# Performance work log

Hardware: AMD Instinct MI355X
Metric: run time of the kernel (lower is better)

Reference implementation:

```python
import jax, jax.numpy as jnp
import numpy as np

N = 50000        # nodes
E = 1600000      # edges (avg degree 32)
F_IN = 512       # input features
HID = 8          # hidden per head (hardcoded in module)
HEADS = 8        # in_head (hardcoded in module)
CLS = 16         # num_classes
NEG_SLOPE = 0.2  # PyG GATConv default


def setup_inputs() -> dict:
    key = jax.random.key(0)
    ks = jax.random.split(key, 12)
    s = 0.05
    return {
        "x": jax.random.normal(ks[0], (N, F_IN), dtype=jnp.float32),
        "edge_index": jax.random.randint(ks[1], (2, E), 0, N, dtype=jnp.int64),
        "W1": jax.random.normal(ks[2], (F_IN, HEADS * HID), dtype=jnp.float32) * s,
        "att_src1": jax.random.normal(ks[3], (HEADS, HID), dtype=jnp.float32) * s,
        "att_dst1": jax.random.normal(ks[4], (HEADS, HID), dtype=jnp.float32) * s,
        "bias1": jax.random.normal(ks[5], (HEADS * HID,), dtype=jnp.float32) * s,
        "W2": jax.random.normal(ks[6], (HEADS * HID, CLS), dtype=jnp.float32) * s,
        "att_src2": jax.random.normal(ks[7], (1, CLS), dtype=jnp.float32) * s,
        "att_dst2": jax.random.normal(ks[8], (1, CLS), dtype=jnp.float32) * s,
        "bias2": jax.random.normal(ks[9], (CLS,), dtype=jnp.float32) * s,
    }


def _gat_conv(x, src, dst, W, att_src, att_dst, bias, n, heads, ch, concat):
    # Linear projection: [n, heads, ch]
    h = (x @ W).reshape(n, heads, ch)
    # Per-node attention logits (PyG style): alpha_src/dst = sum(h * a)
    a_src = jnp.einsum("nhc,hc->nh", h, att_src)  # [n, heads]
    a_dst = jnp.einsum("nhc,hc->nh", h, att_dst)
    # Per-edge raw score, leaky_relu, then segment softmax over incoming edges per dst
    e = jax.nn.leaky_relu(a_src[src] + a_dst[dst], NEG_SLOPE)  # [Etot, heads]
    m = jax.ops.segment_max(e, dst, num_segments=n)            # [n, heads]
    w = jnp.exp(e - m[dst])
    den = jax.ops.segment_sum(w, dst, num_segments=n)
    alpha = w / den[dst]                                        # [Etot, heads]
    # Scatter-aggregate weighted source features
    out = jax.ops.segment_sum(h[src] * alpha[..., None], dst, num_segments=n)  # [n, heads, ch]
    out = out.reshape(n, heads * ch) if concat else out.mean(axis=1)
    return out + bias


def reference(x, edge_index, W1, att_src1, att_dst1, bias1, W2, att_src2, att_dst2, bias2):
    n = x.shape[0]
    # PyG GATConv adds self-loops by default
    loops = jnp.arange(n, dtype=edge_index.dtype)
    src = jnp.concatenate([edge_index[0], loops])
    dst = jnp.concatenate([edge_index[1], loops])
    # dropout(p=0.6) is identity in eval mode
    h = _gat_conv(x, src, dst, W1, att_src1, att_dst1, bias1, n, HEADS, HID, True)
    h = jax.nn.elu(h)
    out = _gat_conv(h, src, dst, W2, att_src2, att_dst2, bias2, n, 1, CLS, False)
    return jax.nn.log_softmax(out, axis=1)
```

## Files before the change

kernel.cpp:

```cpp
#include <hip/hip_runtime.h>
#include <cstddef>

#define N_NODES 50000
#define N_EDGES 1600000
#define N_ETOT  (N_EDGES + N_NODES)
#define F_IN    512
#define HEADS   8
#define HID     8
#define CLS     16

#define NBUCK   196
#define BCAP    12288
#define CHUNKA  4096
#define NB_GEMM1 782
#define NB_BUCKA 391

typedef float v4 __attribute__((ext_vector_type(4)));
typedef float v2 __attribute__((ext_vector_type(2)));
typedef unsigned short us4 __attribute__((ext_vector_type(4)));
typedef unsigned int u4 __attribute__((ext_vector_type(4)));
typedef short bfrag __attribute__((ext_vector_type(8)));
typedef float ffrag __attribute__((ext_vector_type(4)));

__device__ inline float b2f_lo(unsigned int u) { return __uint_as_float(u << 16); }
__device__ inline float b2f_hi(unsigned int u) { return __uint_as_float(u & 0xffff0000u); }
__device__ inline unsigned short f2b(float f) {
  unsigned int x = __float_as_uint(f);
  unsigned int r = (x + 0x7fffu + ((x >> 16) & 1u)) >> 16;
  return (unsigned short)r;
}

__global__ __launch_bounds__(256) void w1t_kernel(
    const float* __restrict__ W, unsigned short* __restrict__ WT,
    int* __restrict__ gcur) {
  int t = threadIdx.x;
  if (blockIdx.x == 128) {
    if (t < NBUCK) gcur[t] = 0;
    return;
  }
  int i = blockIdx.x * 256 + t;
  int k = i >> 6, n = i & 63;
  WT[n * F_IN + k] = f2b(W[i]);
}

__global__ __launch_bounds__(256) void gemm1_bucketA_kernel(
    const float* __restrict__ x, const unsigned short* __restrict__ W1bT,
    const float* __restrict__ att_src, const float* __restrict__ att_dst,
    unsigned short* __restrict__ h1b, float* __restrict__ a_src,
    float* __restrict__ a_dst, int nrows,
    const int* __restrict__ src_idx, const int* __restrict__ dst_idx,
    int* __restrict__ gcur, int* __restrict__ abuck) {
  __shared__ unsigned short xsb[64][72];
  __shared__ unsigned short wsb[64][72];
  __shared__ int hist[NBUCK];
  __shared__ int base[NBUCK];
  __shared__ int cur[NBUCK];
  int t = threadIdx.x;

  if (blockIdx.x >= NB_GEMM1) {
    if (t < NBUCK) hist[t] = 0;
    __syncthreads();
    int blk = blockIdx.x - NB_GEMM1;
    int e0 = blk * CHUNKA;
    int eend = e0 + CHUNKA;
    if (eend > N_EDGES) eend = N_EDGES;
    for (int e = e0 + t; e < eend; e += 256)
      atomicAdd(&hist[(unsigned)dst_idx[e] >> 8], 1);
    __syncthreads();
    if (t < NBUCK) {
      int c = hist[t];
      base[t] = c ? atomicAdd(&gcur[t], c) : 0;
      cur[t] = 0;
    }
    __syncthreads();
    for (int e = e0 + t; e < eend; e += 256) {
      int s = src_idx[e];
      int d = dst_idx[e];
      int b = (unsigned)d >> 8;
      int r = atomicAdd(&cur[b], 1);
      abuck[b * BCAP + base[b] + r] = (s << 8) | (d & 255);
    }
    return;
  }

  int lane = t & 63;
  int w = t >> 6;
  int row0 = blockIdx.x * 64;
  ffrag acc[4];
  acc[0] = 0.f; acc[1] = 0.f; acc[2] = 0.f; acc[3] = 0.f;

  int mrow = lane & 15;
  int koff = (lane >> 4) * 8;

  for (int kt = 0; kt < 8; ++kt) {
    int k0 = kt * 64;
#pragma unroll
    for (int r = 0; r < 4; ++r) {
      int slot = t + r * 256;
      int m = slot >> 4;
      int k4 = (slot & 15) * 4;
      v4 v = 0.f;
      int grow = row0 + m;
      if (grow < nrows) v = *(const v4*)(x + (size_t)grow * F_IN + k0 + k4);
      us4 o;
      o.x = f2b(v[0]); o.y = f2b(v[1]); o.z = f2b(v[2]); o.w = f2b(v[3]);
      *(us4*)&xsb[m][k4] = o;
    }
#pragma unroll
    for (int r = 0; r < 2; ++r) {
      int slot = t + r * 256;
      int nn = slot >> 3;
      int k8 = (slot & 7) * 8;
      *(bfrag*)&wsb[nn][k8] = *(const bfrag*)(W1bT + nn * F_IN + k0 + k8);
    }
    __syncthreads();
#pragma unroll
    for (int kk = 0; kk < 64; kk += 32) {
      bfrag a = *(const bfrag*)&xsb[w * 16 + mrow][kk + koff];
#pragma unroll
      for (int tt = 0; tt < 4; ++tt) {
        bfrag b = *(const bfrag*)&wsb[tt * 16 + mrow][kk + koff];
        acc[tt] = __builtin_amdgcn_mfma_f32_16x16x32_bf16(a, b, acc[tt], 0, 0, 0);
      }
    }
    __syncthreads();
  }
  int c = lane & 15, q = lane >> 4;
  float as_[4], ad_[4];
#pragma unroll
  for (int tt = 0; tt < 4; ++tt) {
    as_[tt] = att_src[tt * 16 + c];
    ad_[tt] = att_dst[tt * 16 + c];
  }
#pragma unroll
  for (int r = 0; r < 4; ++r) {
    int grow = row0 + w * 16 + q * 4 + r;
    float ps[4], pd[4];
#pragma unroll
    for (int tt = 0; tt < 4; ++tt) {
      ps[tt] = acc[tt][r] * as_[tt];
      pd[tt] = acc[tt][r] * ad_[tt];
    }
#pragma unroll
    for (int o = 1; o < 8; o <<= 1) {
#pragma unroll
      for (int tt = 0; tt < 4; ++tt) {
        ps[tt] += __shfl_xor(ps[tt], o);
        pd[tt] += __shfl_xor(pd[tt], o);
      }
    }
    if (grow < nrows) {
#pragma unroll
      for (int tt = 0; tt < 4; ++tt)
        h1b[(size_t)grow * 64 + tt * 16 + c] = f2b(acc[tt][r]);
      if ((c & 7) == 0) {
#pragma unroll
        for (int tt = 0; tt < 4; ++tt) {
          int head = tt * 2 + (c >> 3);
          a_src[grow * 8 + head] = ps[tt];
          a_dst[grow * 8 + head] = pd[tt];
        }
      }
    }
  }
}

__global__ __launch_bounds__(256) void bucketB_kernel(
    const int* __restrict__ gcur, const int* __restrict__ abuck,
    int* __restrict__ indptr, unsigned short* __restrict__ csr16) {
  __shared__ int gs[256];
  __shared__ int hist[256];
  __shared__ int sm[256];
  __shared__ int cur[256];
  int b = blockIdx.x;
  int t = threadIdx.x;
  int gv = (t < NBUCK) ? gcur[t] : 0;
  gs[t] = gv;
  __syncthreads();
  for (int o = 1; o < 256; o <<= 1) {
    int u = (t >= o) ? gs[t - o] : 0;
    __syncthreads();
    gs[t] += u;
    __syncthreads();
  }
  int bbase = (b > 0 ? gs[b - 1] : 0) + 256 * b;
  int M = gcur[b];
  int node0 = b * 256;
  int nnodes = N_NODES - node0;
  if (nnodes > 256) nnodes = 256;
  hist[t] = (t < nnodes) ? 1 : 0;
  __syncthreads();
  const int* ab = abuck + b * BCAP;
  for (int i = t; i < M; i += 256)
    atomicAdd(&hist[ab[i] & 255], 1);
  __syncthreads();
  int v = hist[t];
  sm[t] = v;
  __syncthreads();
  for (int o = 1; o < 256; o <<= 1) {
    int u = (t >= o) ? sm[t - o] : 0;
    __syncthreads();
    sm[t] += u;
    __syncthreads();
  }
  int excl = sm[t] - v;
  cur[t] = excl;
  if (t < nnodes) indptr[node0 + t] = bbase + excl;
  if (b == NBUCK - 1 && t == 0) indptr[N_NODES] = N_ETOT;
  __syncthreads();
  for (int i = t; i < M; i += 256) {
    int entry = ab[i];
    int r = atomicAdd(&cur[entry & 255], 1);
    csr16[bbase + r] = (unsigned short)((unsigned)entry >> 8);
  }
  if (t < nnodes) {
    int r = atomicAdd(&cur[t], 1);
    csr16[bbase + r] = (unsigned short)(node0 + t);
  }
}

__global__ __launch_bounds__(256) void agg1_kernel(
    const int* __restrict__ indptr, const unsigned short* __restrict__ csr16,
    const unsigned short* __restrict__ h1b, const float* __restrict__ a_src1,
    const float* __restrict__ a_dst1, const float* __restrict__ bias1,
    float* __restrict__ h_elu, int n) {
  int wave = threadIdx.x >> 6;
  int lane = threadIdx.x & 63;
  int node = blockIdx.x * 4 + wave;
  if (node >= n) return;
  int j = lane >> 3;
  int h = lane & 7;
  float adst = a_dst1[(unsigned)(node * 8 + h)];
  int beg = indptr[node], end = indptr[node + 1];
  v2 acc[4];
  acc[0] = 0.f; acc[1] = 0.f; acc[2] = 0.f; acc[3] = 0.f;
  float den = 0.f;
  for (int base = beg; base < end; base += 64) {
    int m = end - base;
    if (m > 64) m = 64;
    int sv = (lane < m) ? (int)csr16[base + lane] : 0;
    for (int p = 0; p < m; p += 32) {
      int i0 = p + j, i1 = p + 8 + j, i2 = p + 16 + j, i3 = p + 24 + j;
      int s0 = __shfl(sv, i0);
      int s1 = __shfl(sv, i1);
      int s2 = __shfl(sv, i2);
      int s3 = __shfl(sv, i3);
      bool a0 = i0 < m, a1 = i1 < m, a2 = i2 < m, a3 = i3 < m;
      float g0 = a_src1[(unsigned)(s0 * 8 + h)];
      float g1 = a_src1[(unsigned)(s1 * 8 + h)];
      float g2 = a_src1[(unsigned)(s2 * 8 + h)];
      float g3 = a_src1[(unsigned)(s3 * 8 + h)];
      u4 f0 = *(const u4*)(h1b + (unsigned)(s0 * 64 + h * 8));
      u4 f1 = *(const u4*)(h1b + (unsigned)(s1 * 64 + h * 8));
      u4 f2 = *(const u4*)(h1b + (unsigned)(s2 * 64 + h * 8));
      u4 f3 = *(const u4*)(h1b + (unsigned)(s3 * 64 + h * 8));
      float e0 = g0 + adst, e1 = g1 + adst, e2 = g2 + adst, e3 = g3 + adst;
      e0 = fmaxf(e0, 0.2f * e0); e1 = fmaxf(e1, 0.2f * e1);
      e2 = fmaxf(e2, 0.2f * e2); e3 = fmaxf(e3, 0.2f * e3);
      float w0 = a0 ? __expf(e0) : 0.f;
      float w1 = a1 ? __expf(e1) : 0.f;
      float w2 = a2 ? __expf(e2) : 0.f;
      float w3 = a3 ? __expf(e3) : 0.f;
      den += (w0 + w1) + (w2 + w3);
      v2 w0v, w1v, w2v, w3v;
      w0v[0] = w0; w0v[1] = w0;
      w1v[0] = w1; w1v[1] = w1;
      w2v[0] = w2; w2v[1] = w2;
      w3v[0] = w3; w3v[1] = w3;
      v2 t0, t1, t2, t3;
      t0[0] = b2f_lo(f0.x); t0[1] = b2f_hi(f0.x);
      t1[0] = b2f_lo(f1.x); t1[1] = b2f_hi(f1.x);
      t2[0] = b2f_lo(f2.x); t2[1] = b2f_hi(f2.x);
      t3[0] = b2f_lo(f3.x); t3[1] = b2f_hi(f3.x);
      acc[0] += w0v * t0 + w1v * t1 + w2v * t2 + w3v * t3;
      t0[0] = b2f_lo(f0.y); t0[1] = b2f_hi(f0.y);
      t1[0] = b2f_lo(f1.y); t1[1] = b2f_hi(f1.y);
      t2[0] = b2f_lo(f2.y); t2[1] = b2f_hi(f2.y);
      t3[0] = b2f_lo(f3.y); t3[1] = b2f_hi(f3.y);
      acc[1] += w0v * t0 + w1v * t1 + w2v * t2 + w3v * t3;
      t0[0] = b2f_lo(f0.z); t0[1] = b2f_hi(f0.z);
      t1[0] = b2f_lo(f1.z); t1[1] = b2f_hi(f1.z);
      t2[0] = b2f_lo(f2.z); t2[1] = b2f_hi(f2.z);
      t3[0] = b2f_lo(f3.z); t3[1] = b2f_hi(f3.z);
      acc[2] += w0v * t0 + w1v * t1 + w2v * t2 + w3v * t3;
      t0[0] = b2f_lo(f0.w); t0[1] = b2f_hi(f0.w);
      t1[0] = b2f_lo(f1.w); t1[1] = b2f_hi(f1.w);
      t2[0] = b2f_lo(f2.w); t2[1] = b2f_hi(f2.w);
      t3[0] = b2f_lo(f3.w); t3[1] = b2f_hi(f3.w);
      acc[3] += w0v * t0 + w1v * t1 + w2v * t2 + w3v * t3;
    }
  }
#pragma unroll
  for (int o = 8; o < 64; o <<= 1) {
    den += __shfl_xor(den, o);
#pragma unroll
    for (int i = 0; i < 4; ++i) {
      acc[i][0] += __shfl_xor(acc[i][0], o);
      acc[i][1] += __shfl_xor(acc[i][1], o);
    }
  }
  if (j == 0) {
    float inv = 1.f / den;
    v4 b0 = *(const v4*)(bias1 + h * 8);
    v4 b1 = *(const v4*)(bias1 + h * 8 + 4);
    v4 o0, o1;
    o0[0] = acc[0][0] * inv + b0[0]; o0[1] = acc[0][1] * inv + b0[1];
    o0[2] = acc[1][0] * inv + b0[2]; o0[3] = acc[1][1] * inv + b0[3];
    o1[0] = acc[2][0] * inv + b1[0]; o1[1] = acc[2][1] * inv + b1[1];
    o1[2] = acc[3][0] * inv + b1[2]; o1[3] = acc[3][1] * inv + b1[3];
#pragma unroll
    for (int k = 0; k < 4; ++k) {
      o0[k] = (o0[k] > 0.f) ? o0[k] : (__expf(o0[k]) - 1.f);
      o1[k] = (o1[k] > 0.f) ? o1[k] : (__expf(o1[k]) - 1.f);
    }
    *(v4*)(h_elu + (size_t)node * 64 + h * 8)     = o0;
    *(v4*)(h_elu + (size_t)node * 64 + h * 8 + 4) = o1;
  }
}

__global__ __launch_bounds__(256) void gemm2_kernel(
    const float* __restrict__ h_elu, const float* __restrict__ W2,
    const float* __restrict__ att_src2, const float* __restrict__ att_dst2,
    unsigned short* __restrict__ h2b, float* __restrict__ a_src2,
    float* __restrict__ a_dst2, int n) {
  __shared__ float xs[64][68];
  __shared__ float ws[64][16];
  int t = threadIdx.x;
  int row0 = blockIdx.x * 64;
  {
    int k = t >> 2, c4 = (t & 3) * 4;
    *(v4*)&ws[k][c4] = *(const v4*)(W2 + (size_t)k * 16 + c4);
  }
#pragma unroll
  for (int r = 0; r < 4; ++r) {
    int idx = t + r * 256;
    int m = idx >> 4;
    int c4 = (idx & 15) * 4;
    v4 v = 0.f;
    int grow = row0 + m;
    if (grow < n) v = *(const v4*)(h_elu + (size_t)grow * 64 + c4);
    *(v4*)&xs[m][c4] = v;
  }
  __syncthreads();
  int r = t >> 2, q = t & 3;
  int grow = row0 + r;
  v4 acc = 0.f;
#pragma unroll
  for (int k = 0; k < 64; ++k) {
    acc += xs[r][k] * *(const v4*)&ws[k][q * 4];
  }
  v4 asv = *(const v4*)(att_src2 + q * 4);
  v4 adv = *(const v4*)(att_dst2 + q * 4);
  float ps = acc[0] * asv[0] + acc[1] * asv[1] + acc[2] * asv[2] + acc[3] * asv[3];
  float pd = acc[0] * adv[0] + acc[1] * adv[1] + acc[2] * adv[2] + acc[3] * adv[3];
  ps += __shfl_xor(ps, 1); ps += __shfl_xor(ps, 2);
  pd += __shfl_xor(pd, 1); pd += __shfl_xor(pd, 2);
  if (grow < n) {
    us4 o;
    o.x = f2b(acc[0]); o.y = f2b(acc[1]); o.z = f2b(acc[2]); o.w = f2b(acc[3]);
    *(us4*)(h2b + (size_t)grow * 16 + q * 4) = o;
    if (q == 0) { a_src2[grow] = ps; a_dst2[grow] = pd; }
  }
}

__global__ __launch_bounds__(256) void agg2_kernel(
    const int* __restrict__ indptr, const unsigned short* __restrict__ csr16,
    const unsigned short* __restrict__ h2b, const float* __restrict__ a_src2,
    const float* __restrict__ a_dst2, const float* __restrict__ bias2,
    float* __restrict__ out, int n) {
  int wave = threadIdx.x >> 6;
  int lane = threadIdx.x & 63;
  int node = blockIdx.x * 4 + wave;
  if (node >= n) return;
  int j = lane >> 3;
  int sub = lane & 7;
  float adst = a_dst2[node];
  int beg = indptr[node], end = indptr[node + 1];
  float acc0 = 0.f, acc1 = 0.f, den = 0.f;
  for (int base = beg; base < end; base += 64) {
    int m = end - base;
    if (m > 64) m = 64;
    int sv = (lane < m) ? (int)csr16[base + lane] : 0;
    for (int p = 0; p < m; p += 32) {
      int i0 = p + j, i1 = p + 8 + j, i2 = p + 16 + j, i3 = p + 24 + j;
      int s0 = __shfl(sv, i0);
      int s1 = __shfl(sv, i1);
      int s2 = __shfl(sv, i2);
      int s3 = __shfl(sv, i3);
      bool a0 = i0 < m, a1 = i1 < m, a2 = i2 < m, a3 = i3 < m;
      float g0 = a_src2[(unsigned)s0];
      float g1 = a_src2[(unsigned)s1];
      float g2 = a_src2[(unsigned)s2];
      float g3 = a_src2[(unsigned)s3];
      unsigned f0 = *(const unsigned*)(h2b + (unsigned)(s0 * 16 + sub * 2));
      unsigned f1 = *(const unsigned*)(h2b + (unsigned)(s1 * 16 + sub * 2));
      unsigned f2 = *(const unsigned*)(h2b + (unsigned)(s2 * 16 + sub * 2));
      unsigned f3 = *(const unsigned*)(h2b + (unsigned)(s3 * 16 + sub * 2));
      float e0 = g0 + adst, e1 = g1 + adst, e2 = g2 + adst, e3 = g3 + adst;
      e0 = fmaxf(e0, 0.2f * e0); e1 = fmaxf(e1, 0.2f * e1);
      e2 = fmaxf(e2, 0.2f * e2); e3 = fmaxf(e3, 0.2f * e3);
      float w0 = a0 ? __expf(e0) : 0.f;
      float w1 = a1 ? __expf(e1) : 0.f;
      float w2 = a2 ? __expf(e2) : 0.f;
      float w3 = a3 ? __expf(e3) : 0.f;
      den += (w0 + w1) + (w2 + w3);
      acc0 += w0 * b2f_lo(f0) + w1 * b2f_lo(f1) + w2 * b2f_lo(f2) + w3 * b2f_lo(f3);
      acc1 += w0 * b2f_hi(f0) + w1 * b2f_hi(f1) + w2 * b2f_hi(f2) + w3 * b2f_hi(f3);
    }
  }
#pragma unroll
  for (int o = 8; o < 64; o <<= 1) {
    den  += __shfl_xor(den, o);
    acc0 += __shfl_xor(acc0, o);
    acc1 += __shfl_xor(acc1, o);
  }
  float inv = 1.f / den;
  float v0 = acc0 * inv + bias2[sub * 2];
  float v1 = acc1 * inv + bias2[sub * 2 + 1];
  float mx = fmaxf(v0, v1);
#pragma unroll
  for (int o = 1; o < 8; o <<= 1) mx = fmaxf(mx, __shfl_xor(mx, o));
  float ss = __expf(v0 - mx) + __expf(v1 - mx);
#pragma unroll
  for (int o = 1; o < 8; o <<= 1) ss += __shfl_xor(ss, o);
  float lg = mx + __logf(ss);
  if (j == 0) {
    v2 r;
    r[0] = v0 - lg;
    r[1] = v1 - lg;
    *(v2*)(out + (size_t)node * 16 + sub * 2) = r;
  }
}

extern "C" void kernel_launch(void* const* d_in, const int* in_sizes, int n_in,
                              void* d_out, int out_size, void* d_ws, size_t ws_size,
                              hipStream_t stream) {
  const float* x        = (const float*)d_in[0];
  const int*   ei       = (const int*)d_in[1];
  const float* W1       = (const float*)d_in[2];
  const float* att_src1 = (const float*)d_in[3];
  const float* att_dst1 = (const float*)d_in[4];
  const float* bias1    = (const float*)d_in[5];
  const float* W2       = (const float*)d_in[6];
  const float* att_src2 = (const float*)d_in[7];
  const float* att_dst2 = (const float*)d_in[8];
  const float* bias2    = (const float*)d_in[9];
  const int* src_idx = ei;
  const int* dst_idx = ei + N_EDGES;

  char* p = (char*)d_ws;
  auto alloc = [&](size_t bytes) {
    void* r = (void*)p;
    p += (bytes + 255) & ~(size_t)255;
    return r;
  };
  unsigned short* h1b = (unsigned short*)alloc((size_t)N_NODES * 64 * 2);
  float* h_elu   = (float*)alloc((size_t)N_NODES * 64 * 4);
  float* a_src1  = (float*)alloc((size_t)N_NODES * 8 * 4);
  float* a_dst1  = (float*)alloc((size_t)N_NODES * 8 * 4);
  unsigned short* h2b = (unsigned short*)alloc((size_t)N_NODES * 16 * 2);
  float* a_src2  = (float*)alloc((size_t)N_NODES * 4);
  float* a_dst2  = (float*)alloc((size_t)N_NODES * 4);
  int* indptr    = (int*)alloc((size_t)(N_NODES + 1) * 4);
  int* gcur      = (int*)alloc((size_t)NBUCK * 4);
  unsigned short* csr16 = (unsigned short*)alloc((size_t)N_ETOT * 2);
  unsigned short* W1bT  = (unsigned short*)alloc((size_t)64 * F_IN * 2);
  int* abuck     = (int*)h_elu;

  w1t_kernel<<<129, 256, 0, stream>>>(W1, W1bT, gcur);

  gemm1_bucketA_kernel<<<NB_GEMM1 + NB_BUCKA, 256, 0, stream>>>(
      x, W1bT, att_src1, att_dst1, h1b, a_src1, a_dst1, N_NODES,
      src_idx, dst_idx, gcur, abuck);

  bucketB_kernel<<<NBUCK, 256, 0, stream>>>(gcur, abuck, indptr, csr16);

  agg1_kernel<<<N_NODES / 4, 256, 0, stream>>>(
      indptr, csr16, h1b, a_src1, a_dst1, bias1, h_elu, N_NODES);

  gemm2_kernel<<<(N_NODES + 63) / 64, 256, 0, stream>>>(
      h_elu, W2, att_src2, att_dst2, h2b, a_src2, a_dst2, N_NODES);

  agg2_kernel<<<N_NODES / 4, 256, 0, stream>>>(
      indptr, csr16, h2b, a_src2, a_dst2, bias2, (float*)d_out, N_NODES);
}
```

Baseline: 282.7 us.

## Load GEMM1 MFMA fragments directly from global memory, dropping LDS staging

Rewrites the first-layer projection GEMM so each lane loads its x row slice and W1 fragments straight from global memory into registers, converting to bf16 in-register. This removes the shared-memory tiles and both __syncthreads per K step. In exchange, the x loads become less coalesced: each lane reads 32-byte strided pieces of its own row. W fragments are now re-read by every wave instead of shared, relying on cache.

Result: slower. 291.9 us (+3.3%).

```diff
diff --git a/kernel.cpp b/kernel.cpp
--- a/kernel.cpp
+++ b/kernel.cpp
@@ -50,8 +50,6 @@
     float* __restrict__ a_dst, int nrows,
     const int* __restrict__ src_idx, const int* __restrict__ dst_idx,
     int* __restrict__ gcur, int* __restrict__ abuck) {
-  __shared__ unsigned short xsb[64][72];
-  __shared__ unsigned short wsb[64][72];
   __shared__ int hist[NBUCK];
   __shared__ int base[NBUCK];
   __shared__ int cur[NBUCK];
@@ -86,45 +84,40 @@
   int lane = t & 63;
   int w = t >> 6;
   int row0 = blockIdx.x * 64;
+  int mrow = lane & 15;
+  int koff = (lane >> 4) * 8;
+
+  int arow = row0 + w * 16 + mrow;
+  if (arow >= nrows) arow = nrows - 1;
+  const float* xrow = x + (size_t)arow * F_IN + koff;
+  const unsigned short* wp0 = W1bT + (size_t)(0 * 16 + mrow) * F_IN + koff;
+  const unsigned short* wp1 = W1bT + (size_t)(1 * 16 + mrow) * F_IN + koff;
+  const unsigned short* wp2 = W1bT + (size_t)(2 * 16 + mrow) * F_IN + koff;
+  const unsigned short* wp3 = W1bT + (size_t)(3 * 16 + mrow) * F_IN + koff;
+
   ffrag acc[4];
   acc[0] = 0.f; acc[1] = 0.f; acc[2] = 0.f; acc[3] = 0.f;
 
-  int mrow = lane & 15;
-  int koff = (lane >> 4) * 8;
-
-  for (int kt = 0; kt < 8; ++kt) {
-    int k0 = kt * 64;
-#pragma unroll
-    for (int r = 0; r < 4; ++r) {
-      int slot = t + r * 256;
-      int m = slot >> 4;
-      int k4 = (slot & 15) * 4;
-      v4 v = 0.f;
-      int grow = row0 + m;
-      if (grow < nrows) v = *(const v4*)(x + (size_t)grow * F_IN + k0 + k4);
-      us4 o;
-      o.x = f2b(v[0]); o.y = f2b(v[1]); o.z = f2b(v[2]); o.w = f2b(v[3]);
-      *(us4*)&xsb[m][k4] = o;
-    }
-#pragma unroll
-    for (int r = 0; r < 2; ++r) {
-      int slot = t + r * 256;
-      int nn = slot >> 3;
-      int k8 = (slot & 7) * 8;
-      *(bfrag*)&wsb[nn][k8] = *(const bfrag*)(W1bT + nn * F_IN + k0 + k8);
-    }
-    __syncthreads();
-#pragma unroll
-    for (int kk = 0; kk < 64; kk += 32) {
-      bfrag a = *(const bfrag*)&xsb[w * 16 + mrow][kk + koff];
-#pragma unroll
-      for (int tt = 0; tt < 4; ++tt) {
-        bfrag b = *(const bfrag*)&wsb[tt * 16 + mrow][kk + koff];
-        acc[tt] = __builtin_amdgcn_mfma_f32_16x16x32_bf16(a, b, acc[tt], 0, 0, 0);
-      }
-    }
-    __syncthreads();
-  }
+#pragma unroll 4
+  for (int kc = 0; kc < 16; ++kc) {
+    int ko = kc * 32;
+    v4 xa = *(const v4*)(xrow + ko);
+    v4 xb = *(const v4*)(xrow + ko + 4);
+    bfrag b0 = *(const bfrag*)(wp0 + ko);
+    bfrag b1 = *(const bfrag*)(wp1 + ko);
+    bfrag b2 = *(const bfrag*)(wp2 + ko);
+    bfrag b3 = *(const bfrag*)(wp3 + ko);
+    bfrag a;
+    a[0] = (short)f2b(xa[0]); a[1] = (short)f2b(xa[1]);
+    a[2] = (short)f2b(xa[2]); a[3] = (short)f2b(xa[3]);
+    a[4] = (short)f2b(xb[0]); a[5] = (short)f2b(xb[1]);
+    a[6] = (short)f2b(xb[2]); a[7] = (short)f2b(xb[3]);
+    acc[0] = __builtin_amdgcn_mfma_f32_16x16x32_bf16(a, b0, acc[0], 0, 0, 0);
+    acc[1] = __builtin_amdgcn_mfma_f32_16x16x32_bf16(a, b1, acc[1], 0, 0, 0);
+    acc[2] = __builtin_amdgcn_mfma_f32_16x16x32_bf16(a, b2, acc[2], 0, 0, 0);
+    acc[3] = __builtin_amdgcn_mfma_f32_16x16x32_bf16(a, b3, acc[3], 0, 0, 0);
+  }
+
   int c = lane & 15, q = lane >> 4;
   float as_[4], ad_[4];
 #pragma unroll
```
